# Kernel optimization log

Measured on AMD Instinct MI355X. Metric: run time of the kernel, lower is better.

Reference implementation:

```python
import jax, jax.numpy as jnp
import numpy as np

N = 8192
F_IN = 256
F_OUT = 128
ALPHA = 0.2  # LeakyReLU negative slope (cfg.model.gat_alpha)


def setup_inputs() -> dict:
    key = jax.random.key(0)
    k1, k2, k3, k4 = jax.random.split(key, 4)
    inp = jax.random.normal(k1, (N, F_IN), dtype=jnp.float32)
    adj = jax.random.randint(k2, (N, N), 0, 2, dtype=jnp.int32)
    # xavier_uniform with gain=1.414
    gain = 1.414
    limW = gain * np.sqrt(6.0 / (F_IN + F_OUT))
    W = jax.random.uniform(k3, (F_IN, F_OUT), minval=-limW, maxval=limW, dtype=jnp.float32)
    lima = gain * np.sqrt(6.0 / (2 * F_OUT + 1))
    a = jax.random.uniform(k4, (2 * F_OUT, 1), minval=-lima, maxval=lima, dtype=jnp.float32)
    return {"input": inp, "adj": adj, "W": W, "a": a}


def reference(input, adj, W, a):
    h = input @ W                     # [N, F_OUT]
    a1 = a[:F_OUT, 0]                 # score contribution of source node i
    a2 = a[F_OUT:, 0]                 # score contribution of target node j
    # e[i, j] = leakyrelu(a1.h_i + a2.h_j)  -- same math as the NxN concat
    s1 = h @ a1                       # [N]
    s2 = h @ a2                       # [N]
    e = jax.nn.leaky_relu(s1[:, None] + s2[None, :], negative_slope=ALPHA)  # [N, N]
    attention = jnp.where(adj > 0, e, jnp.float32(-9e15))
    attention = jax.nn.softmax(attention, axis=1)
    # dropout p=0 / eval mode -> no-op
    h_prime = attention @ h           # [N, F_OUT]
    return jax.nn.elu(h_prime)        # concat=True branch
```

## Files before the change

kernel.cpp:

```cpp
#include <hip/hip_runtime.h>
#include <hip/hip_bf16.h>

#define N 8192
#define FIN 256
#define FOUT 128
#define ALPHA 0.2f

typedef unsigned short ushort_t;
typedef __attribute__((ext_vector_type(8))) short short8;
typedef __attribute__((ext_vector_type(4))) float f32x4;

#define GLOAD16(gp, lp)                                        \
  __builtin_amdgcn_global_load_lds(                            \
      (const __attribute__((address_space(1))) void*)(gp),     \
      (__attribute__((address_space(3))) void*)(lp), 16, 0, 0)

__device__ __forceinline__ ushort_t f2bf(float x) {
  __hip_bfloat16 b = __float2bfloat16(x);
  return *reinterpret_cast<ushort_t*>(&b);
}

__global__ __launch_bounds__(256) void k_h(const float* __restrict__ inp,
                                           const float* __restrict__ Wm,
                                           const float* __restrict__ av,
                                           ushort_t* __restrict__ hT,
                                           float* __restrict__ s1,
                                           float* __restrict__ s2) {
  __shared__ float in_lds[16][FIN];
  __shared__ float h_tile[16][FOUT];
  const int t = threadIdx.x;
  const int r0 = blockIdx.x * 16;

  for (int idx = t; idx < 16 * FIN; idx += 256) {
    int ii = idx >> 8, kk = idx & 255;
    in_lds[ii][kk] = inp[(size_t)(r0 + ii) * FIN + kk];
  }
  __syncthreads();

  const int c2 = (t & 63) * 2;
  const int rg = t >> 6;
  float acc[4][2] = {};
  for (int k = 0; k < FIN; k += 4) {
    float4 iv[4];
#pragma unroll
    for (int q = 0; q < 4; ++q)
      iv[q] = *reinterpret_cast<const float4*>(&in_lds[rg * 4 + q][k]);
#pragma unroll
    for (int kk = 0; kk < 4; ++kk) {
      float2 wp = *reinterpret_cast<const float2*>(&Wm[(size_t)(k + kk) * FOUT + c2]);
#pragma unroll
      for (int q = 0; q < 4; ++q) {
        float x = reinterpret_cast<const float*>(&iv[q])[kk];
        acc[q][0] = fmaf(x, wp.x, acc[q][0]);
        acc[q][1] = fmaf(x, wp.y, acc[q][1]);
      }
    }
  }
#pragma unroll
  for (int q = 0; q < 4; ++q) {
    h_tile[rg * 4 + q][c2] = acc[q][0];
    h_tile[rg * 4 + q][c2 + 1] = acc[q][1];
  }
  __syncthreads();

  const int wv_ = t >> 6, lane = t & 63;
#pragma unroll
  for (int rr = 0; rr < 4; ++rr) {
    int row = wv_ * 4 + rr;
    float h0 = h_tile[row][lane], h1 = h_tile[row][lane + 64];
    float p1 = h0 * av[lane] + h1 * av[lane + 64];
    float p2 = h0 * av[FOUT + lane] + h1 * av[FOUT + lane + 64];
#pragma unroll
    for (int m = 32; m; m >>= 1) {
      p1 += __shfl_xor(p1, m);
      p2 += __shfl_xor(p2, m);
    }
    if (lane == 0) { s1[r0 + row] = p1; s2[r0 + row] = p2; }
  }

  for (int idx = t; idx < 16 * FOUT; idx += 256) {
    int c = idx >> 4, ii = idx & 15;
    hT[(size_t)c * N + r0 + ii] = f2bf(h_tile[ii][c]);
  }
}

__global__ __launch_bounds__(256) void k_smax(const float* __restrict__ s2,
                                              float* __restrict__ outm) {
  __shared__ float red[4];
  const int t = threadIdx.x;
  float m = -1e30f;
  for (int i = t; i < N; i += 256) m = fmaxf(m, s2[i]);
#pragma unroll
  for (int d = 32; d; d >>= 1) m = fmaxf(m, __shfl_xor(m, d));
  if ((t & 63) == 0) red[t >> 6] = m;
  __syncthreads();
  if (t == 0) outm[0] = fmaxf(fmaxf(red[0], red[1]), fmaxf(red[2], red[3]));
}

__global__ __launch_bounds__(512, 4) void k_attn(const int* __restrict__ adj,
                                                 const ushort_t* __restrict__ hT,
                                                 const float* __restrict__ s1g,
                                                 const float* __restrict__ s2g,
                                                 const float* __restrict__ s2max,
                                                 float* __restrict__ slab,
                                                 float* __restrict__ denp,
                                                 int jc, int ntiles) {
  __shared__ __align__(16) ushort_t Bt[32768];
  __shared__ float Dred[8][16];

  const int t = threadIdx.x;
  const int lane = t & 63;
  const int wid = t >> 6;
  const int rb = blockIdx.x & 127;
  const int chunk = blockIdx.x >> 7;
  const int i0 = rb * 64;
  const int jc0 = chunk * jc;

  const int g = wid & 3;
  const int hf = wid >> 2;
  const int arow = lane & 15;
  const int kb = lane >> 4;
  const int irow = i0 + g * 16 + arow;

  const float s1v = s1g[irow];
  const float mraw = s1v + s2max[0];
  const float mv = mraw > 0.f ? mraw : ALPHA * mraw;
  const float L2E = 1.44269504f;
  const float mvl = mv * L2E;

  const int* __restrict__ adjp = adj + (size_t)irow * N + jc0 + hf * 128 + kb * 8;
  const float* __restrict__ s2p = s2g + jc0 + hf * 128 + kb * 8;
  const char* __restrict__ hTb = (const char*)hT;

  f32x4 acc[8];
#pragma unroll
  for (int ct = 0; ct < 8; ++ct) acc[ct] = (f32x4){0.f, 0.f, 0.f, 0.f};
  float dacc = 0.f;

  for (int jt = 0; jt < ntiles; ++jt) {
    const int j0 = jt * 256;

#pragma unroll
    for (int s = 0; s < 8; ++s) {
      int L = s * 512 + t;
      int row = L >> 5;
      int boff = (L & 31) * 16;
      const char* src = hTb + ((size_t)row * N + jc0 + j0) * 2 + (boff ^ ((row & 7) << 4));
      GLOAD16(src, (char*)Bt + L * 16);
    }

    int4 a0[4], a1[4];
#pragma unroll
    for (int kq = 0; kq < 4; ++kq) {
      a0[kq] = *reinterpret_cast<const int4*>(adjp + j0 + kq * 32);
      a1[kq] = *reinterpret_cast<const int4*>(adjp + j0 + kq * 32 + 4);
    }

    __syncthreads();

#pragma unroll
    for (int kq = 0; kq < 4; ++kq) {
      short8 bf[8];
      const int byte0 = hf * 256 + kq * 64 + kb * 16;
#pragma unroll
      for (int ct = 0; ct < 8; ++ct) {
        int row = ct * 16 + arow;
        int off = row * 512 + (byte0 ^ ((row & 7) << 4));
        bf[ct] = *reinterpret_cast<const short8*>((const char*)Bt + off);
      }
      float4 sv0 = *reinterpret_cast<const float4*>(s2p + j0 + kq * 32);
      float4 sv1 = *reinterpret_cast<const float4*>(s2p + j0 + kq * 32 + 4);
      const int* ai0 = reinterpret_cast<const int*>(&a0[kq]);
      const int* ai1 = reinterpret_cast<const int*>(&a1[kq]);
      const float* sf0 = reinterpret_cast<const float*>(&sv0);
      const float* sf1 = reinterpret_cast<const float*>(&sv1);
      short8 af;
#pragma unroll
      for (int e = 0; e < 4; ++e) {
        float pre = s1v + sf0[e];
        float lr = fmaxf(pre, ALPHA * pre);
        float w = __builtin_amdgcn_exp2f(fmaf(lr, L2E, -mvl));
        w = (ai0[e] > 0) ? w : 0.f;
        dacc += w;
        af[e] = (short)f2bf(w);
      }
#pragma unroll
      for (int e = 0; e < 4; ++e) {
        float pre = s1v + sf1[e];
        float lr = fmaxf(pre, ALPHA * pre);
        float w = __builtin_amdgcn_exp2f(fmaf(lr, L2E, -mvl));
        w = (ai1[e] > 0) ? w : 0.f;
        dacc += w;
        af[4 + e] = (short)f2bf(w);
      }
#pragma unroll
      for (int ct = 0; ct < 8; ++ct)
        acc[ct] = __builtin_amdgcn_mfma_f32_16x16x32_bf16(af, bf[ct], acc[ct], 0, 0, 0);
    }

    __syncthreads();
  }

  dacc += __shfl_xor(dacc, 16);
  dacc += __shfl_xor(dacc, 32);
  if (lane < 16) Dred[wid][lane] = dacc;

  float (*Hred)[132] = (float(*)[132])(void*)Bt;
  if (hf == 0) {
#pragma unroll
    for (int ct = 0; ct < 8; ++ct)
#pragma unroll
      for (int r = 0; r < 4; ++r)
        Hred[g * 16 + kb * 4 + r][ct * 16 + arow] = acc[ct][r];
  }
  __syncthreads();
  if (hf == 1) {
#pragma unroll
    for (int ct = 0; ct < 8; ++ct)
#pragma unroll
      for (int r = 0; r < 4; ++r)
        Hred[g * 16 + kb * 4 + r][ct * 16 + arow] += acc[ct][r];
  }
  __syncthreads();

  if (t < 64)
    denp[(size_t)chunk * N + i0 + t] = Dred[t >> 4][t & 15] + Dred[(t >> 4) + 4][t & 15];

  for (int idx = t; idx < 64 * 128; idx += 512) {
    int r = idx >> 7, c = idx & 127;
    slab[((size_t)chunk * N + i0 + r) * 128 + c] = Hred[r][c];
  }
}

__global__ __launch_bounds__(256) void k_fin(const float* __restrict__ slab,
                                             const float* __restrict__ denp,
                                             float* __restrict__ out, int nchunks) {
  const int idx = blockIdx.x * 256 + threadIdx.x;
  const int i = idx >> 7;
  float den = 0.f, v = 0.f;
  for (int k = 0; k < nchunks; ++k) {
    den += denp[(size_t)k * N + i];
    v += slab[(size_t)k * N * FOUT + idx];
  }
  v /= den;
  out[idx] = v > 0.f ? v : (__expf(v) - 1.f);
}

extern "C" void kernel_launch(void* const* d_in, const int* in_sizes, int n_in,
                              void* d_out, int out_size, void* d_ws, size_t ws_size,
                              hipStream_t stream) {
  const float* inp = (const float*)d_in[0];
  const int* adj   = (const int*)d_in[1];
  const float* Wm  = (const float*)d_in[2];
  const float* av  = (const float*)d_in[3];
  float* out = (float*)d_out;

  char* ws = (char*)d_ws;
  ushort_t* hT = (ushort_t*)ws;
  float* s1    = (float*)(ws + (size_t)FOUT * N * 2);
  float* s2    = s1 + N;
  float* s2mx  = s2 + N;
  float* slab  = s2mx + 4;

  const size_t base = (size_t)FOUT * N * 2 + (size_t)N * 4 * 2 + 16;
  int nchunks = 4;
  while (nchunks > 1) {
    size_t need = base + (size_t)nchunks * N * FOUT * 4 + (size_t)nchunks * N * 4;
    if (need <= ws_size) break;
    nchunks >>= 1;
  }
  float* denp = slab + (size_t)nchunks * N * FOUT;
  const int jc = N / nchunks;
  const int ntiles = jc / 256;

  k_h<<<N / 16, 256, 0, stream>>>(inp, Wm, av, hT, s1, s2);
  k_smax<<<1, 256, 0, stream>>>(s2, s2mx);
  k_attn<<<128 * nchunks, 512, 0, stream>>>(adj, hT, s1, s2, s2mx, slab, denp, jc, ntiles);
  k_fin<<<(N * FOUT) / 256, 256, 0, stream>>>(slab, denp, out, nchunks);
}
```

Before: 125.7 us.

## Pack adjacency into bitmask and register-stage double-buffer hT tiles

Adds a pre-pass kernel that compresses the int32 adjacency matrix into a row-major bitmask, so the attention kernel reads one bit per edge instead of four bytes. It also replaces the direct global-to-LDS loads of hT with register prefetch of the next tile that is written to LDS after compute, overlapping global latency with MFMA work. The full adjacency still has to be read once by the pack kernel, so total traffic barely drops, and the extra launch plus register pressure from the prefetch buffers may offset the gains.

```diff
diff --git a/kernel.cpp b/kernel.cpp
--- a/kernel.cpp
+++ b/kernel.cpp
@@ -10,14 +10,29 @@
 typedef __attribute__((ext_vector_type(8))) short short8;
 typedef __attribute__((ext_vector_type(4))) float f32x4;
 
-#define GLOAD16(gp, lp)                                        \
-  __builtin_amdgcn_global_load_lds(                            \
-      (const __attribute__((address_space(1))) void*)(gp),     \
-      (__attribute__((address_space(3))) void*)(lp), 16, 0, 0)
-
 __device__ __forceinline__ ushort_t f2bf(float x) {
   __hip_bfloat16 b = __float2bfloat16(x);
   return *reinterpret_cast<ushort_t*>(&b);
+}
+
+__global__ __launch_bounds__(256) void k_pack(const int* __restrict__ adj,
+                                              unsigned* __restrict__ maskRM) {
+  const size_t tid = (size_t)blockIdx.x * 256 + threadIdx.x;
+  const size_t nthr = (size_t)gridDim.x * 256;
+  const size_t nwords = (size_t)N * (N / 32);
+  for (size_t w = tid; w < nwords; w += nthr) {
+    const int4* p = reinterpret_cast<const int4*>(adj + w * 32);
+    unsigned m = 0;
+#pragma unroll
+    for (int s = 0; s < 8; ++s) {
+      int4 v = p[s];
+      m |= (v.x > 0 ? 1u : 0u) << (s * 4);
+      m |= (v.y > 0 ? 1u : 0u) << (s * 4 + 1);
+      m |= (v.z > 0 ? 1u : 0u) << (s * 4 + 2);
+      m |= (v.w > 0 ? 1u : 0u) << (s * 4 + 3);
+    }
+    maskRM[w] = m;
+  }
 }
 
 __global__ __launch_bounds__(256) void k_h(const float* __restrict__ inp,
@@ -97,7 +112,7 @@
   if (t == 0) outm[0] = fmaxf(fmaxf(red[0], red[1]), fmaxf(red[2], red[3]));
 }
 
-__global__ __launch_bounds__(512, 4) void k_attn(const int* __restrict__ adj,
+__global__ __launch_bounds__(512, 4) void k_attn(const unsigned* __restrict__ maskRM,
                                                  const ushort_t* __restrict__ hT,
                                                  const float* __restrict__ s1g,
                                                  const float* __restrict__ s2g,
@@ -128,35 +143,46 @@
   const float L2E = 1.44269504f;
   const float mvl = mv * L2E;
 
-  const int* __restrict__ adjp = adj + (size_t)irow * N + jc0 + hf * 128 + kb * 8;
+  const unsigned* __restrict__ maskp =
+      maskRM + (size_t)irow * (N / 32) + ((jc0 + hf * 128) >> 5);
   const float* __restrict__ s2p = s2g + jc0 + hf * 128 + kb * 8;
   const char* __restrict__ hTb = (const char*)hT;
 
+  int4* const BtV = reinterpret_cast<int4*>(Bt);
+
+#define ISSUE(J0)                                                                   \
+  {                                                                                 \
+    _Pragma("unroll") for (int s = 0; s < 8; ++s) {                                 \
+      int L = s * 512 + t;                                                          \
+      int rr = L >> 5;                                                              \
+      int boff = (L & 31) * 16;                                                     \
+      const char* src =                                                             \
+          hTb + ((size_t)rr * N + jc0 + (J0)) * 2 + (boff ^ ((rr & 7) << 4));       \
+      hrg[s] = *reinterpret_cast<const int4*>(src);                                 \
+    }                                                                               \
+  }
+
+#define WRITE_STAGE()                                                               \
+  {                                                                                 \
+    _Pragma("unroll") for (int s = 0; s < 8; ++s) BtV[s * 512 + t] = hrg[s];        \
+  }
+
   f32x4 acc[8];
 #pragma unroll
   for (int ct = 0; ct < 8; ++ct) acc[ct] = (f32x4){0.f, 0.f, 0.f, 0.f};
   float dacc = 0.f;
+  int4 hrg[8];
+
+  ISSUE(0)
+  WRITE_STAGE()
+  __syncthreads();
 
   for (int jt = 0; jt < ntiles; ++jt) {
     const int j0 = jt * 256;
 
-#pragma unroll
-    for (int s = 0; s < 8; ++s) {
-      int L = s * 512 + t;
-      int row = L >> 5;
-      int boff = (L & 31) * 16;
-      const char* src = hTb + ((size_t)row * N + jc0 + j0) * 2 + (boff ^ ((row & 7) << 4));
-      GLOAD16(src, (char*)Bt + L * 16);
-    }
-
-    int4 a0[4], a1[4];
-#pragma unroll
-    for (int kq = 0; kq < 4; ++kq) {
-      a0[kq] = *reinterpret_cast<const int4*>(adjp + j0 + kq * 32);
-      a1[kq] = *reinterpret_cast<const int4*>(adjp + j0 + kq * 32 + 4);
-    }
-
-    __syncthreads();
+    if (jt + 1 < ntiles) ISSUE((jt + 1) * 256)
+
+    int4 mw = *reinterpret_cast<const int4*>(maskp + (j0 >> 5));
 
 #pragma unroll
     for (int kq = 0; kq < 4; ++kq) {
@@ -168,10 +194,10 @@
         int off = row * 512 + (byte0 ^ ((row & 7) << 4));
         bf[ct] = *reinterpret_cast<const short8*>((const char*)Bt + off);
       }
+      const unsigned word = (kq == 0) ? mw.x : (kq == 1) ? mw.y : (kq == 2) ? mw.z : mw.w;
+      const unsigned w8 = (word >> (kb * 8)) & 0xffu;
       float4 sv0 = *reinterpret_cast<const float4*>(s2p + j0 + kq * 32);
       float4 sv1 = *reinterpret_cast<const float4*>(s2p + j0 + kq * 32 + 4);
-      const int* ai0 = reinterpret_cast<const int*>(&a0[kq]);
-      const int* ai1 = reinterpret_cast<const int*>(&a1[kq]);
       const float* sf0 = reinterpret_cast<const float*>(&sv0);
       const float* sf1 = reinterpret_cast<const float*>(&sv1);
       short8 af;
@@ -180,7 +206,7 @@
         float pre = s1v + sf0[e];
         float lr = fmaxf(pre, ALPHA * pre);
         float w = __builtin_amdgcn_exp2f(fmaf(lr, L2E, -mvl));
-        w = (ai0[e] > 0) ? w : 0.f;
+        w = ((w8 >> e) & 1u) ? w : 0.f;
         dacc += w;
         af[e] = (short)f2bf(w);
       }
@@ -189,7 +215,7 @@
         float pre = s1v + sf1[e];
         float lr = fmaxf(pre, ALPHA * pre);
         float w = __builtin_amdgcn_exp2f(fmaf(lr, L2E, -mvl));
-        w = (ai1[e] > 0) ? w : 0.f;
+        w = ((w8 >> (4 + e)) & 1u) ? w : 0.f;
         dacc += w;
         af[4 + e] = (short)f2bf(w);
       }
@@ -199,13 +225,20 @@
     }
 
     __syncthreads();
-  }
+    if (jt + 1 < ntiles) {
+      WRITE_STAGE()
+      __syncthreads();
+    }
+  }
+#undef ISSUE
+#undef WRITE_STAGE
 
   dacc += __shfl_xor(dacc, 16);
   dacc += __shfl_xor(dacc, 32);
   if (lane < 16) Dred[wid][lane] = dacc;
 
   float (*Hred)[132] = (float(*)[132])(void*)Bt;
+  __syncthreads();
   if (hf == 0) {
 #pragma unroll
     for (int ct = 0; ct < 8; ++ct)
@@ -260,9 +293,10 @@
   float* s1    = (float*)(ws + (size_t)FOUT * N * 2);
   float* s2    = s1 + N;
   float* s2mx  = s2 + N;
-  float* slab  = s2mx + 4;
-
-  const size_t base = (size_t)FOUT * N * 2 + (size_t)N * 4 * 2 + 16;
+  unsigned* maskRM = (unsigned*)(s2mx + 4);
+  float* slab  = (float*)(maskRM + (size_t)N * N / 32);
+
+  const size_t base = (size_t)FOUT * N * 2 + (size_t)N * 4 * 2 + 16 + (size_t)N * N / 8;
   int nchunks = 4;
   while (nchunks > 1) {
     size_t need = base + (size_t)nchunks * N * FOUT * 4 + (size_t)nchunks * N * 4;
@@ -273,8 +307,9 @@
   const int jc = N / nchunks;
   const int ntiles = jc / 256;
 
+  k_pack<<<2048, 256, 0, stream>>>(adj, maskRM);
   k_h<<<N / 16, 256, 0, stream>>>(inp, Wm, av, hT, s1, s2);
   k_smax<<<1, 256, 0, stream>>>(s2, s2mx);
-  k_attn<<<128 * nchunks, 512, 0, stream>>>(adj, hT, s1, s2, s2mx, slab, denp, jc, ntiles);
+  k_attn<<<128 * nchunks, 512, 0, stream>>>(maskRM, hT, s1, s2, s2mx, slab, denp, jc, ntiles);
   k_fin<<<(N * FOUT) / 256, 256, 0, stream>>>(slab, denp, out, nchunks);
 }
```

New measurement: 249.0 us. 1.98x slower.
